# Kernel optimization log

Hardware: AMD Instinct MI355X
Metric: run time of the kernel (lower is better)

## Reference

```python
import jax, jax.numpy as jnp
import numpy as np

P, G, F, H = 128, 256, 1024, 512
EPS = 1e-5

def _bn(x, g, b, m, v):
    # eval-mode BatchNorm1d over last dim
    return (x - m) / jnp.sqrt(v + EPS) * g + b

def _lrelu(x):
    return jnp.where(x > 0, x, 0.1 * x)

def setup_inputs():
    key = jax.random.key(0)
    ks = iter(jax.random.split(key, 64))
    rn = lambda s, sc=1.0: jax.random.normal(next(ks), s, dtype=jnp.float32) * sc
    ru = lambda s: jax.random.uniform(next(ks), s, dtype=jnp.float32) + 0.5
    return {
        "f_p": rn((P, F)), "f_g": rn((G, F)),
        "bn_g": ru((F,)), "bn_b": rn((F,), 0.1), "bn_m": rn((F,), 0.1), "bn_v": ru((F,)),
        "rf_W1": rn((F, F), 0.02), "rf_b1": rn((F,), 0.01),
        "rf1_g": ru((F,)), "rf1_b": rn((F,), 0.1), "rf1_m": rn((F,), 0.1), "rf1_v": ru((F,)),
        "rf_W2": rn((F, F), 0.02), "rf_b2": rn((F,), 0.01),
        "rf2_g": ru((F,)), "rf2_b": rn((F,), 0.1), "rf2_m": rn((F,), 0.1), "rf2_v": ru((F,)),
        "sfc_W": rn((F, H), 0.02), "sfc_b": rn((H,), 0.01),
        "sbn_g": ru((H,)), "sbn_b": rn((H,), 0.1), "sbn_m": rn((H,), 0.1), "sbn_v": ru((H,)),
        "scl_W": rn((H, 1), 0.001), "scl_b": rn((1,), 0.001),
        "ffc_W": rn((F, H), 0.02), "ffc_b": rn((H,), 0.01),
        "fbn_g": ru((H,)), "fbn_b": rn((H,), 0.1), "fbn_m": rn((H,), 0.1), "fbn_v": ru((H,)),
        "cls_W": rn((H, 1), 0.001), "cls_b": rn((1,), 0.001),
    }

def reference(f_p, f_g, bn_g, bn_b, bn_m, bn_v,
              rf_W1, rf_b1, rf1_g, rf1_b, rf1_m, rf1_v,
              rf_W2, rf_b2, rf2_g, rf2_b, rf2_m, rf2_v,
              sfc_W, sfc_b, sbn_g, sbn_b, sbn_m, sbn_v, scl_W, scl_b,
              ffc_W, ffc_b, fbn_g, fbn_b, fbn_m, fbn_v, cls_W, cls_b):
    # Siamese difference feature for every probe-gallery pair: d [P,G,F]
    d = _bn((f_p[:, None, :] - f_g[None, :, :]) ** 2, bn_g, bn_b, bn_m, bn_v)
    h = _lrelu(_bn(d @ rf_W1 + rf_b1, rf1_g, rf1_b, rf1_m, rf1_v))
    t = _lrelu(_bn(h @ rf_W2 + rf_b2, rf2_g, rf2_b, rf2_m, rf2_v))
    # Gallery-gallery scalar affinities via Siamese FcBlock + ClassBlock: w [G,G]
    dg = _bn((f_g[:, None, :] - f_g[None, :, :]) ** 2, bn_g, bn_b, bn_m, bn_v)
    hg = _lrelu(_bn(dg @ sfc_W + sfc_b, sbn_g, sbn_b, sbn_m, sbn_v))
    w = (hg @ scl_W + scl_b)[..., 0]
    # Graph diffusion over the gallery axis: d_new = t @ w  [P,G,F]
    d_new = jnp.einsum('pgf,gh->phf', t, w)
    # Per-pair FC + classifier -> scalar score per (probe, gallery) pair
    feat = _lrelu(_bn(d_new @ ffc_W + ffc_b, fbn_g, fbn_b, fbn_m, fbn_v))
    result = (feat @ cls_W + cls_b)[..., 0]
    return result
```

## Files before the change

kernel.cpp:

```cpp
#include <hip/hip_runtime.h>


typedef __bf16 bf16;
typedef __attribute__((ext_vector_type(8))) __bf16 bf16x8;
typedef __attribute__((ext_vector_type(4))) float f32x4;

#define EPSV 1e-5f

__device__ __forceinline__ void async_load16(const bf16* g, bf16* l) {
    __builtin_amdgcn_global_load_lds(
        (const __attribute__((address_space(1))) void*)g,
        (__attribute__((address_space(3))) void*)l, 16, 0, 0);
}

__global__ __launch_bounds__(256) void prep_kernel(
    const float* __restrict__ g, const float* __restrict__ b,
    const float* __restrict__ m, const float* __restrict__ v,
    const float* __restrict__ bias, float* __restrict__ scale,
    float* __restrict__ offset, int n)
{
    int i = blockIdx.x * 256 + threadIdx.x;
    if (i >= n) return;
    float s = g[i] / sqrtf(v[i] + EPSV);
    float o = b[i] - m[i] * s;
    if (bias) o += bias[i] * s;
    scale[i] = s;
    offset[i] = o;
}

__global__ __launch_bounds__(256) void wtrans_kernel(
    const float* __restrict__ in, bf16* __restrict__ out, int K, int N)
{
    int k = blockIdx.x * 256 + threadIdx.x;
    int n = blockIdx.y;
    out[(size_t)n * K + k] = (bf16)in[(size_t)k * N + n];
}

__global__ __launch_bounds__(256) void wconv_kernel(
    const float* __restrict__ w_acc, const float* __restrict__ sclb,
    bf16* __restrict__ wT)
{
    int tid = blockIdx.x * 256 + threadIdx.x;
    int g2 = tid >> 8, g1 = tid & 255;
    int idx = ((g1 >> 4) <= (g2 >> 4)) ? (g1 * 256 + g2) : (g2 * 256 + g1);
    wT[tid] = (bf16)(w_acc[idx] + sclb[0]);
}

__global__ __launch_bounds__(256) void utrans_kernel(
    const bf16* __restrict__ u, bf16* __restrict__ uT)
{
    __shared__ float tile[64][65];
    int g0 = blockIdx.x * 64, h0 = blockIdx.y * 64, p = blockIdx.z;
    const bf16* up = u + (size_t)p * 256 * 512;
    bf16* op = uT + (size_t)p * 512 * 256;
    for (int c = threadIdx.x; c < 512; c += 256) {
        int r = c >> 3, hc = (c & 7) * 8;
        bf16x8 val = *(const bf16x8*)(up + (size_t)(g0 + r) * 512 + h0 + hc);
#pragma unroll
        for (int j = 0; j < 8; ++j) tile[r][hc + j] = (float)val[j];
    }
    __syncthreads();
    for (int c = threadIdx.x; c < 512; c += 256) {
        int hr = c >> 3, gc = (c & 7) * 8;
        bf16x8 val;
#pragma unroll
        for (int j = 0; j < 8; ++j) val[j] = (bf16)tile[gc + j][hr];
        *(bf16x8*)(op + (size_t)(h0 + hr) * 256 + g0 + gc) = val;
    }
}

__global__ __launch_bounds__(256) void finout_kernel(
    const float* __restrict__ acc, const float* __restrict__ clsb,
    float* __restrict__ out)
{
    int i = blockIdx.x * 256 + threadIdx.x;
    out[i] = acc[i] + clsb[0];
}

__global__ __launch_bounds__(512) void gemm256(
    const bf16* __restrict__ A,
    const float* __restrict__ pairX, const float* __restrict__ pairY,
    const float* __restrict__ ps, const float* __restrict__ po,
    const bf16* __restrict__ BT,
    bf16* __restrict__ C,
    int K, int N, int rowOff,
    const float* __restrict__ scale, const float* __restrict__ offset,
    int lrelu)
{
    __shared__ bf16 As[256 * 64];
    __shared__ bf16 Bs[256 * 64];
    const int tid  = threadIdx.x;
    const int lane = tid & 63;
    const int wave = tid >> 6;
    const int wrow = wave >> 2, wcol = wave & 3;
    const int row0 = blockIdx.y * 256;
    const int col0 = blockIdx.x * 256;
    const int q = lane >> 4, l16 = lane & 15;

    f32x4 acc[8][4];
#pragma unroll
    for (int mi = 0; mi < 8; ++mi)
#pragma unroll
        for (int ni = 0; ni < 4; ++ni)
#pragma unroll
            for (int e = 0; e < 4; ++e) acc[mi][ni][e] = 0.f;

    for (int kk = 0; kk < K; kk += 64) {
        if (pairX) {
#pragma unroll
            for (int t = 0; t < 4; ++t) {
                int c = tid + t * 512;
                int r = c >> 3, ch = c & 7;
                int gr = rowOff + row0 + r;
                const float* xp = pairX + (size_t)(gr >> 8) * K + kk + ch * 8;
                const float* yp = pairY + (size_t)(gr & 255) * K + kk + ch * 8;
                f32x4 x0 = *(const f32x4*)xp, x1 = *(const f32x4*)(xp + 4);
                f32x4 y0 = *(const f32x4*)yp, y1 = *(const f32x4*)(yp + 4);
                f32x4 sa = *(const f32x4*)(ps + kk + ch * 8);
                f32x4 sb = *(const f32x4*)(ps + kk + ch * 8 + 4);
                f32x4 oa = *(const f32x4*)(po + kk + ch * 8);
                f32x4 ob = *(const f32x4*)(po + kk + ch * 8 + 4);
                bf16x8 dv;
#pragma unroll
                for (int j = 0; j < 4; ++j) {
                    float d0 = x0[j] - y0[j];
                    float d1 = x1[j] - y1[j];
                    dv[j]     = (bf16)(d0 * d0 * sa[j] + oa[j]);
                    dv[j + 4] = (bf16)(d1 * d1 * sb[j] + ob[j]);
                }
                *(bf16x8*)&As[r * 64 + ((ch ^ (r & 7)) * 8)] = dv;
            }
        } else {
#pragma unroll
            for (int t = 0; t < 4; ++t) {
                int idx = t * 512 + tid;
                int r = idx >> 3, sch = idx & 7;
                int gch = sch ^ (r & 7);
                async_load16(A + (size_t)(row0 + r) * K + kk + gch * 8,
                             &As[idx * 8]);
            }
        }
#pragma unroll
        for (int t = 0; t < 4; ++t) {
            int idx = t * 512 + tid;
            int r = idx >> 3, sch = idx & 7;
            int gch = sch ^ (r & 7);
            async_load16(BT + (size_t)(col0 + r) * K + kk + gch * 8,
                         &Bs[idx * 8]);
        }
        __syncthreads();

#pragma unroll
        for (int s = 0; s < 2; ++s) {
            bf16x8 af[8], bfr[4];
#pragma unroll
            for (int mi = 0; mi < 8; ++mi) {
                int r = wrow * 128 + mi * 16 + l16;
                af[mi] = *(const bf16x8*)&As[r * 64 + (((s * 4 + q) ^ (r & 7)) * 8)];
            }
#pragma unroll
            for (int ni = 0; ni < 4; ++ni) {
                int rc = wcol * 64 + ni * 16 + l16;
                bfr[ni] = *(const bf16x8*)&Bs[rc * 64 + (((s * 4 + q) ^ (rc & 7)) * 8)];
            }
#pragma unroll
            for (int mi = 0; mi < 8; ++mi)
#pragma unroll
                for (int ni = 0; ni < 4; ++ni)
                    acc[mi][ni] = __builtin_amdgcn_mfma_f32_16x16x32_bf16(
                        af[mi], bfr[ni], acc[mi][ni], 0, 0, 0);
        }
        __syncthreads();
    }

#pragma unroll
    for (int mi = 0; mi < 8; ++mi)
#pragma unroll
        for (int ni = 0; ni < 4; ++ni)
#pragma unroll
            for (int i = 0; i < 4; ++i) {
                int r = row0 + wrow * 128 + mi * 16 + q * 4 + i;
                int cc = col0 + wcol * 64 + ni * 16 + l16;
                float val = acc[mi][ni][i];
                if (scale) val = val * scale[cc] + offset[cc];
                if (lrelu) val = val > 0.f ? val : 0.1f * val;
                C[(size_t)r * N + cc] = (bf16)val;
            }
}

__global__ __launch_bounds__(512) void gemm_aff(
    const float* __restrict__ pairX,
    const float* __restrict__ ps, const float* __restrict__ po,
    const bf16* __restrict__ BT,
    int K,
    const float* __restrict__ scale, const float* __restrict__ offset,
    const float* __restrict__ sclW, float* __restrict__ w_acc)
{
    __shared__ bf16 As[256 * 64];
    __shared__ bf16 Bs[128 * 64];
    const int tid  = threadIdx.x;
    const int lane = tid & 63;
    const int wave = tid >> 6;
    const int wrow = wave >> 1, wcol = wave & 1;
    const int q = lane >> 4, l16 = lane & 15;
    const int col0 = blockIdx.x * 128;

    int ta = 0, rem = blockIdx.y;
    while (rem >= 16 - ta) { rem -= 16 - ta; ++ta; }
    const int tb = ta + rem;

    f32x4 acc[4][4];
#pragma unroll
    for (int mi = 0; mi < 4; ++mi)
#pragma unroll
        for (int ni = 0; ni < 4; ++ni)
#pragma unroll
            for (int e = 0; e < 4; ++e) acc[mi][ni][e] = 0.f;

    for (int kk = 0; kk < K; kk += 64) {
#pragma unroll
        for (int t = 0; t < 4; ++t) {
            int c = tid + t * 512;
            int r = c >> 3, ch = c & 7;
            int g1 = ta * 16 + (r >> 4), g2 = tb * 16 + (r & 15);
            const float* xp = pairX + (size_t)g1 * K + kk + ch * 8;
            const float* yp = pairX + (size_t)g2 * K + kk + ch * 8;
            f32x4 x0 = *(const f32x4*)xp, x1 = *(const f32x4*)(xp + 4);
            f32x4 y0 = *(const f32x4*)yp, y1 = *(const f32x4*)(yp + 4);
            f32x4 sa = *(const f32x4*)(ps + kk + ch * 8);
            f32x4 sb = *(const f32x4*)(ps + kk + ch * 8 + 4);
            f32x4 oa = *(const f32x4*)(po + kk + ch * 8);
            f32x4 ob = *(const f32x4*)(po + kk + ch * 8 + 4);
            bf16x8 dv;
#pragma unroll
            for (int j = 0; j < 4; ++j) {
                float d0 = x0[j] - y0[j];
                float d1 = x1[j] - y1[j];
                dv[j]     = (bf16)(d0 * d0 * sa[j] + oa[j]);
                dv[j + 4] = (bf16)(d1 * d1 * sb[j] + ob[j]);
            }
            *(bf16x8*)&As[r * 64 + ((ch ^ (r & 7)) * 8)] = dv;
        }
#pragma unroll
        for (int t = 0; t < 2; ++t) {
            int idx = t * 512 + tid;
            int r = idx >> 3, sch = idx & 7;
            int gch = sch ^ (r & 7);
            async_load16(BT + (size_t)(col0 + r) * K + kk + gch * 8,
                         &Bs[idx * 8]);
        }
        __syncthreads();

#pragma unroll
        for (int s = 0; s < 2; ++s) {
            bf16x8 af[4], bfr[4];
#pragma unroll
            for (int mi = 0; mi < 4; ++mi) {
                int r = wrow * 64 + mi * 16 + l16;
                af[mi] = *(const bf16x8*)&As[r * 64 + (((s * 4 + q) ^ (r & 7)) * 8)];
            }
#pragma unroll
            for (int ni = 0; ni < 4; ++ni) {
                int rc = wcol * 64 + ni * 16 + l16;
                bfr[ni] = *(const bf16x8*)&Bs[rc * 64 + (((s * 4 + q) ^ (rc & 7)) * 8)];
            }
#pragma unroll
            for (int mi = 0; mi < 4; ++mi)
#pragma unroll
                for (int ni = 0; ni < 4; ++ni)
                    acc[mi][ni] = __builtin_amdgcn_mfma_f32_16x16x32_bf16(
                        af[mi], bfr[ni], acc[mi][ni], 0, 0, 0);
        }
        __syncthreads();
    }

#pragma unroll
    for (int mi = 0; mi < 4; ++mi)
#pragma unroll
        for (int i = 0; i < 4; ++i) {
            float rs = 0.f;
#pragma unroll
            for (int ni = 0; ni < 4; ++ni) {
                int cc = col0 + wcol * 64 + ni * 16 + l16;
                float val = acc[mi][ni][i] * scale[cc] + offset[cc];
                val = val > 0.f ? val : 0.1f * val;
                rs += val * sclW[cc];
            }
            rs += __shfl_xor(rs, 1, 64);
            rs += __shfl_xor(rs, 2, 64);
            rs += __shfl_xor(rs, 4, 64);
            rs += __shfl_xor(rs, 8, 64);
            if (l16 == 0) {
                int r = wrow * 64 + mi * 16 + q * 4 + i;
                int g1 = ta * 16 + (r >> 4), g2 = tb * 16 + (r & 15);
                atomicAdd(w_acc + g1 * 256 + g2, rs);
            }
        }
}

__global__ __launch_bounds__(256) void gemm_kernel(
    const bf16* __restrict__ A,
    const bf16* __restrict__ BT, bf16* __restrict__ C,
    int K, int N, long long batchB, long long batchC,
    const float* __restrict__ scale, const float* __restrict__ offset,
    int lrelu, const float* __restrict__ fuseW, float* __restrict__ facc,
    long long faccStride)
{
    __shared__ bf16 As[128 * 64];
    __shared__ bf16 Bs[128 * 64];
    const int tid  = threadIdx.x;
    const int lane = tid & 63;
    const int wave = tid >> 6;
    const int wr = wave >> 1, wc = wave & 1;
    const int row0 = blockIdx.y * 128;
    const int col0 = blockIdx.x * 128;
    const int q = lane >> 4, l16 = lane & 15;
    const int drow = lane >> 3;
    const int dsch = lane & 7;

    const bf16* Bp = BT + (size_t)blockIdx.z * (size_t)batchB;
    bf16* Cp = C + (size_t)blockIdx.z * (size_t)batchC;

    f32x4 acc[4][4];
#pragma unroll
    for (int mi = 0; mi < 4; ++mi)
#pragma unroll
        for (int ni = 0; ni < 4; ++ni)
#pragma unroll
            for (int e = 0; e < 4; ++e) acc[mi][ni][e] = 0.f;

    for (int kk = 0; kk < K; kk += 64) {
#pragma unroll
        for (int t = 0; t < 4; ++t) {
            int grp = wave * 4 + t;
            int r = grp * 8 + drow;
            int gch = dsch ^ (r & 7);
            async_load16(A + (size_t)(row0 + r) * K + kk + gch * 8,
                         &As[grp * 512 + lane * 8]);
        }
#pragma unroll
        for (int t = 0; t < 4; ++t) {
            int grp = wave * 4 + t;
            int r = grp * 8 + drow;
            int gch = dsch ^ (r & 7);
            async_load16(Bp + (size_t)(col0 + r) * K + kk + gch * 8,
                         &Bs[grp * 512 + lane * 8]);
        }
        __syncthreads();
#pragma unroll
        for (int s = 0; s < 2; ++s) {
            bf16x8 af[4], bfr[4];
#pragma unroll
            for (int mi = 0; mi < 4; ++mi) {
                int r = wr * 64 + mi * 16 + l16;
                af[mi] = *(const bf16x8*)&As[r * 64 + (((s * 4 + q) ^ (r & 7)) * 8)];
            }
#pragma unroll
            for (int ni = 0; ni < 4; ++ni) {
                int rc = wc * 64 + ni * 16 + l16;
                bfr[ni] = *(const bf16x8*)&Bs[rc * 64 + (((s * 4 + q) ^ (rc & 7)) * 8)];
            }
#pragma unroll
            for (int mi = 0; mi < 4; ++mi)
#pragma unroll
                for (int ni = 0; ni < 4; ++ni)
                    acc[mi][ni] = __builtin_amdgcn_mfma_f32_16x16x32_bf16(
                        af[mi], bfr[ni], acc[mi][ni], 0, 0, 0);
        }
        __syncthreads();
    }

    if (fuseW) {
#pragma unroll
        for (int mi = 0; mi < 4; ++mi)
#pragma unroll
            for (int i = 0; i < 4; ++i) {
                float rs = 0.f;
#pragma unroll
                for (int ni = 0; ni < 4; ++ni) {
                    int cc = col0 + wc * 64 + ni * 16 + l16;
                    float val = acc[mi][ni][i] * scale[cc] + offset[cc];
                    val = val > 0.f ? val : 0.1f * val;
                    rs += val * fuseW[cc];
                }
                rs += __shfl_xor(rs, 1, 64);
                rs += __shfl_xor(rs, 2, 64);
                rs += __shfl_xor(rs, 4, 64);
                rs += __shfl_xor(rs, 8, 64);
                if (l16 == 0) {
                    int r = row0 + wr * 64 + mi * 16 + q * 4 + i;
                    atomicAdd(facc + (size_t)blockIdx.z * faccStride + r, rs);
                }
            }
        return;
    }
#pragma unroll
    for (int mi = 0; mi < 4; ++mi)
#pragma unroll
        for (int ni = 0; ni < 4; ++ni)
#pragma unroll
            for (int i = 0; i < 4; ++i) {
                int r = row0 + wr * 64 + mi * 16 + q * 4 + i;
                int cc = col0 + wc * 64 + ni * 16 + l16;
                float val = acc[mi][ni][i];
                if (scale) val = val * scale[cc] + offset[cc];
                if (lrelu) val = val > 0.f ? val : 0.1f * val;
                Cp[(size_t)r * N + cc] = (bf16)val;
            }
}

extern "C" void kernel_launch(void* const* d_in, const int* in_sizes, int n_in,
                              void* d_out, int out_size, void* d_ws, size_t ws_size,
                              hipStream_t stream)
{
    const float* f_p   = (const float*)d_in[0];
    const float* f_g   = (const float*)d_in[1];
    const float* bn_g  = (const float*)d_in[2];
    const float* bn_b  = (const float*)d_in[3];
    const float* bn_m  = (const float*)d_in[4];
    const float* bn_v  = (const float*)d_in[5];
    const float* rf_W1 = (const float*)d_in[6];
    const float* rf_b1 = (const float*)d_in[7];
    const float* rf1_g = (const float*)d_in[8];
    const float* rf1_b = (const float*)d_in[9];
    const float* rf1_m = (const float*)d_in[10];
    const float* rf1_v = (const float*)d_in[11];
    const float* rf_W2 = (const float*)d_in[12];
    const float* rf_b2 = (const float*)d_in[13];
    const float* rf2_g = (const float*)d_in[14];
    const float* rf2_b = (const float*)d_in[15];
    const float* rf2_m = (const float*)d_in[16];
    const float* rf2_v = (const float*)d_in[17];
    const float* sfc_W = (const float*)d_in[18];
    const float* sfc_b = (const float*)d_in[19];
    const float* sbn_g = (const float*)d_in[20];
    const float* sbn_b = (const float*)d_in[21];
    const float* sbn_m = (const float*)d_in[22];
    const float* sbn_v = (const float*)d_in[23];
    const float* scl_W = (const float*)d_in[24];
    const float* scl_b = (const float*)d_in[25];
    const float* ffc_W = (const float*)d_in[26];
    const float* ffc_b = (const float*)d_in[27];
    const float* fbn_g = (const float*)d_in[28];
    const float* fbn_b = (const float*)d_in[29];
    const float* fbn_m = (const float*)d_in[30];
    const float* fbn_v = (const float*)d_in[31];
    const float* cls_W = (const float*)d_in[32];
    const float* cls_b = (const float*)d_in[33];

    const size_t MB = 1ull << 20;
    char* ws = (char*)d_ws;
    float* SC      = (float*)(ws);
    float *s0 = SC,        *o0 = SC + 1024;
    float *s1 = SC + 2048, *o1 = SC + 3072;
    float *s2 = SC + 4096, *o2 = SC + 5120;
    float *s3 = SC + 6144, *o3 = SC + 6656;
    float *s4 = SC + 7168, *o4 = SC + 7680;
    float* w_acc   = (float*)(ws + 65536);
    float* out_acc = (float*)(ws + 327680);
    bf16* wT       = (bf16*)(ws + 458752);
    bf16* W1T      = (bf16*)(ws + 1 * MB);
    bf16* W2T      = (bf16*)(ws + 3 * MB);
    bf16* sfcT     = (bf16*)(ws + 5 * MB);
    bf16* ffcT     = (bf16*)(ws + 6 * MB);

    int nc;
    if      (ws_size >= 170 * MB) nc = 1;
    else if (ws_size >= 90 * MB)  nc = 2;
    else                          nc = 4;
    const int pc = 128 / nc;
    const int R  = pc * 256;
    const size_t hbytes = (size_t)R * 1024 * 2;
    bf16* bufA = (bf16*)(ws + 8 * MB);
    bf16* bufB = (bf16*)(ws + 8 * MB + hbytes);
    bf16* bufC = (bf16*)(ws + 8 * MB + 2 * hbytes);

    prep_kernel<<<dim3(4), 256, 0, stream>>>(bn_g, bn_b, bn_m, bn_v, nullptr, s0, o0, 1024);
    prep_kernel<<<dim3(4), 256, 0, stream>>>(rf1_g, rf1_b, rf1_m, rf1_v, rf_b1, s1, o1, 1024);
    prep_kernel<<<dim3(4), 256, 0, stream>>>(rf2_g, rf2_b, rf2_m, rf2_v, rf_b2, s2, o2, 1024);
    prep_kernel<<<dim3(2), 256, 0, stream>>>(sbn_g, sbn_b, sbn_m, sbn_v, sfc_b, s3, o3, 512);
    prep_kernel<<<dim3(2), 256, 0, stream>>>(fbn_g, fbn_b, fbn_m, fbn_v, ffc_b, s4, o4, 512);

    wtrans_kernel<<<dim3(4, 1024), 256, 0, stream>>>(rf_W1, W1T, 1024, 1024);
    wtrans_kernel<<<dim3(4, 1024), 256, 0, stream>>>(rf_W2, W2T, 1024, 1024);
    wtrans_kernel<<<dim3(4, 512), 256, 0, stream>>>(sfc_W, sfcT, 1024, 512);
    wtrans_kernel<<<dim3(4, 512), 256, 0, stream>>>(ffc_W, ffcT, 1024, 512);

    hipMemsetAsync(ws + 65536, 0, 393216, stream);

    gemm_aff<<<dim3(4, 136), 512, 0, stream>>>(
        f_g, s0, o0, sfcT, 1024, s3, o3, scl_W, w_acc);
    wconv_kernel<<<dim3(256), 256, 0, stream>>>(w_acc, scl_b, wT);

    for (int ci = 0; ci < nc; ++ci) {
        gemm256<<<dim3(4, R / 256), 512, 0, stream>>>(
            nullptr, f_p, f_g, s0, o0, W1T, bufA, 1024, 1024, ci * R,
            s1, o1, 1);
        gemm256<<<dim3(4, R / 256), 512, 0, stream>>>(
            bufA, nullptr, nullptr, nullptr, nullptr, W2T, bufB, 1024, 1024, 0,
            s2, o2, 1);
        gemm256<<<dim3(2, R / 256), 512, 0, stream>>>(
            bufB, nullptr, nullptr, nullptr, nullptr, ffcT, bufC, 1024, 512, 0,
            nullptr, nullptr, 0);
        utrans_kernel<<<dim3(4, 8, pc), 256, 0, stream>>>(bufC, bufA);
        gemm_kernel<<<dim3(4, 2, pc), 256, 0, stream>>>(
            wT, bufA, nullptr, 256, 512, (long long)512 * 256, 0,
            s4, o4, 1, cls_W, out_acc + (size_t)ci * pc * 256, 256);
    }
    finout_kernel<<<dim3(128), 256, 0, stream>>>(out_acc, cls_b, (float*)d_out);
}
```

Baseline: 592.2 us.

## Compute transposed FFC output directly and drop the transpose kernel

The FFC GEMM is recast as ffcT × bufB^T per probe, batched over the probe axis, so it writes the [H,G] layout the diffusion GEMM needs directly. This removes the separate utrans transpose kernel and its extra global round trip. gemm256 gains batch strides and a fused BN+LReLU+classifier row-reduction epilogue, replacing the smaller 128-tile gemm_kernel for the diffusion step. The diffusion GEMM now launches far fewer, larger blocks (2×1×pc), which may lower occupancy.

Result: faster. 566.7 us (-4.3%).

```diff
diff --git a/kernel.cpp b/kernel.cpp
--- a/kernel.cpp
+++ b/kernel.cpp
@@ -46,29 +46,6 @@
     wT[tid] = (bf16)(w_acc[idx] + sclb[0]);
 }
 
-__global__ __launch_bounds__(256) void utrans_kernel(
-    const bf16* __restrict__ u, bf16* __restrict__ uT)
-{
-    __shared__ float tile[64][65];
-    int g0 = blockIdx.x * 64, h0 = blockIdx.y * 64, p = blockIdx.z;
-    const bf16* up = u + (size_t)p * 256 * 512;
-    bf16* op = uT + (size_t)p * 512 * 256;
-    for (int c = threadIdx.x; c < 512; c += 256) {
-        int r = c >> 3, hc = (c & 7) * 8;
-        bf16x8 val = *(const bf16x8*)(up + (size_t)(g0 + r) * 512 + h0 + hc);
-#pragma unroll
-        for (int j = 0; j < 8; ++j) tile[r][hc + j] = (float)val[j];
-    }
-    __syncthreads();
-    for (int c = threadIdx.x; c < 512; c += 256) {
-        int hr = c >> 3, gc = (c & 7) * 8;
-        bf16x8 val;
-#pragma unroll
-        for (int j = 0; j < 8; ++j) val[j] = (bf16)tile[gc + j][hr];
-        *(bf16x8*)(op + (size_t)(h0 + hr) * 256 + g0 + gc) = val;
-    }
-}
-
 __global__ __launch_bounds__(256) void finout_kernel(
     const float* __restrict__ acc, const float* __restrict__ clsb,
     float* __restrict__ out)
@@ -84,8 +61,11 @@
     const bf16* __restrict__ BT,
     bf16* __restrict__ C,
     int K, int N, int rowOff,
+    long long batchA, long long batchB, long long batchC,
     const float* __restrict__ scale, const float* __restrict__ offset,
-    int lrelu)
+    int lrelu,
+    const float* __restrict__ fuseW, float* __restrict__ facc,
+    long long faccStride)
 {
     __shared__ bf16 As[256 * 64];
     __shared__ bf16 Bs[256 * 64];
@@ -96,6 +76,10 @@
     const int row0 = blockIdx.y * 256;
     const int col0 = blockIdx.x * 256;
     const int q = lane >> 4, l16 = lane & 15;
+    const int z = blockIdx.z;
+
+    const bf16* Ap = A + (size_t)z * (size_t)batchA;
+    const bf16* Bp = BT + (size_t)z * (size_t)batchB;
 
     f32x4 acc[8][4];
 #pragma unroll
@@ -136,7 +120,7 @@
                 int idx = t * 512 + tid;
                 int r = idx >> 3, sch = idx & 7;
                 int gch = sch ^ (r & 7);
-                async_load16(A + (size_t)(row0 + r) * K + kk + gch * 8,
+                async_load16(Ap + (size_t)(row0 + r) * K + kk + gch * 8,
                              &As[idx * 8]);
             }
         }
@@ -145,7 +129,7 @@
             int idx = t * 512 + tid;
             int r = idx >> 3, sch = idx & 7;
             int gch = sch ^ (r & 7);
-            async_load16(BT + (size_t)(col0 + r) * K + kk + gch * 8,
+            async_load16(Bp + (size_t)(col0 + r) * K + kk + gch * 8,
                          &Bs[idx * 8]);
         }
         __syncthreads();
@@ -173,6 +157,31 @@
         __syncthreads();
     }
 
+    if (fuseW) {
+#pragma unroll
+        for (int mi = 0; mi < 8; ++mi)
+#pragma unroll
+            for (int i = 0; i < 4; ++i) {
+                float rs = 0.f;
+#pragma unroll
+                for (int ni = 0; ni < 4; ++ni) {
+                    int cc = col0 + wcol * 64 + ni * 16 + l16;
+                    float val = acc[mi][ni][i] * scale[cc] + offset[cc];
+                    val = val > 0.f ? val : 0.1f * val;
+                    rs += val * fuseW[cc];
+                }
+                rs += __shfl_xor(rs, 1, 64);
+                rs += __shfl_xor(rs, 2, 64);
+                rs += __shfl_xor(rs, 4, 64);
+                rs += __shfl_xor(rs, 8, 64);
+                if (l16 == 0) {
+                    int r = row0 + wrow * 128 + mi * 16 + q * 4 + i;
+                    atomicAdd(facc + (size_t)z * faccStride + r, rs);
+                }
+            }
+        return;
+    }
+    bf16* Cp = C + (size_t)z * (size_t)batchC;
 #pragma unroll
     for (int mi = 0; mi < 8; ++mi)
 #pragma unroll
@@ -184,7 +193,7 @@
                 float val = acc[mi][ni][i];
                 if (scale) val = val * scale[cc] + offset[cc];
                 if (lrelu) val = val > 0.f ? val : 0.1f * val;
-                C[(size_t)r * N + cc] = (bf16)val;
+                Cp[(size_t)r * N + cc] = (bf16)val;
             }
 }
 
@@ -296,117 +305,6 @@
                 atomicAdd(w_acc + g1 * 256 + g2, rs);
             }
         }
-}
-
-__global__ __launch_bounds__(256) void gemm_kernel(
-    const bf16* __restrict__ A,
-    const bf16* __restrict__ BT, bf16* __restrict__ C,
-    int K, int N, long long batchB, long long batchC,
-    const float* __restrict__ scale, const float* __restrict__ offset,
-    int lrelu, const float* __restrict__ fuseW, float* __restrict__ facc,
-    long long faccStride)
-{
-    __shared__ bf16 As[128 * 64];
-    __shared__ bf16 Bs[128 * 64];
-    const int tid  = threadIdx.x;
-    const int lane = tid & 63;
-    const int wave = tid >> 6;
-    const int wr = wave >> 1, wc = wave & 1;
-    const int row0 = blockIdx.y * 128;
-    const int col0 = blockIdx.x * 128;
-    const int q = lane >> 4, l16 = lane & 15;
-    const int drow = lane >> 3;
-    const int dsch = lane & 7;
-
-    const bf16* Bp = BT + (size_t)blockIdx.z * (size_t)batchB;
-    bf16* Cp = C + (size_t)blockIdx.z * (size_t)batchC;
-
-    f32x4 acc[4][4];
-#pragma unroll
-    for (int mi = 0; mi < 4; ++mi)
-#pragma unroll
-        for (int ni = 0; ni < 4; ++ni)
-#pragma unroll
-            for (int e = 0; e < 4; ++e) acc[mi][ni][e] = 0.f;
-
-    for (int kk = 0; kk < K; kk += 64) {
-#pragma unroll
-        for (int t = 0; t < 4; ++t) {
-            int grp = wave * 4 + t;
-            int r = grp * 8 + drow;
-            int gch = dsch ^ (r & 7);
-            async_load16(A + (size_t)(row0 + r) * K + kk + gch * 8,
-                         &As[grp * 512 + lane * 8]);
-        }
-#pragma unroll
-        for (int t = 0; t < 4; ++t) {
-            int grp = wave * 4 + t;
-            int r = grp * 8 + drow;
-            int gch = dsch ^ (r & 7);
-            async_load16(Bp + (size_t)(col0 + r) * K + kk + gch * 8,
-                         &Bs[grp * 512 + lane * 8]);
-        }
-        __syncthreads();
-#pragma unroll
-        for (int s = 0; s < 2; ++s) {
-            bf16x8 af[4], bfr[4];
-#pragma unroll
-            for (int mi = 0; mi < 4; ++mi) {
-                int r = wr * 64 + mi * 16 + l16;
-                af[mi] = *(const bf16x8*)&As[r * 64 + (((s * 4 + q) ^ (r & 7)) * 8)];
-            }
-#pragma unroll
-            for (int ni = 0; ni < 4; ++ni) {
-                int rc = wc * 64 + ni * 16 + l16;
-                bfr[ni] = *(const bf16x8*)&Bs[rc * 64 + (((s * 4 + q) ^ (rc & 7)) * 8)];
-            }
-#pragma unroll
-            for (int mi = 0; mi < 4; ++mi)
-#pragma unroll
-                for (int ni = 0; ni < 4; ++ni)
-                    acc[mi][ni] = __builtin_amdgcn_mfma_f32_16x16x32_bf16(
-                        af[mi], bfr[ni], acc[mi][ni], 0, 0, 0);
-        }
-        __syncthreads();
-    }
-
-    if (fuseW) {
-#pragma unroll
-        for (int mi = 0; mi < 4; ++mi)
-#pragma unroll
-            for (int i = 0; i < 4; ++i) {
-                float rs = 0.f;
-#pragma unroll
-                for (int ni = 0; ni < 4; ++ni) {
-                    int cc = col0 + wc * 64 + ni * 16 + l16;
-                    float val = acc[mi][ni][i] * scale[cc] + offset[cc];
-                    val = val > 0.f ? val : 0.1f * val;
-                    rs += val * fuseW[cc];
-                }
-                rs += __shfl_xor(rs, 1, 64);
-                rs += __shfl_xor(rs, 2, 64);
-                rs += __shfl_xor(rs, 4, 64);
-                rs += __shfl_xor(rs, 8, 64);
-                if (l16 == 0) {
-                    int r = row0 + wr * 64 + mi * 16 + q * 4 + i;
-                    atomicAdd(facc + (size_t)blockIdx.z * faccStride + r, rs);
-                }
-            }
-        return;
-    }
-#pragma unroll
-    for (int mi = 0; mi < 4; ++mi)
-#pragma unroll
-        for (int ni = 0; ni < 4; ++ni)
-#pragma unroll
-            for (int i = 0; i < 4; ++i) {
-                int r = row0 + wr * 64 + mi * 16 + q * 4 + i;
-                int cc = col0 + wc * 64 + ni * 16 + l16;
-                float val = acc[mi][ni][i];
-                if (scale) val = val * scale[cc] + offset[cc];
-                if (lrelu) val = val > 0.f ? val : 0.1f * val;
-                Cp[(size_t)r * N + cc] = (bf16)val;
-            }
 }
 
 extern "C" void kernel_launch(void* const* d_in, const int* in_sizes, int n_in,
@@ -495,16 +393,17 @@
     for (int ci = 0; ci < nc; ++ci) {
         gemm256<<<dim3(4, R / 256), 512, 0, stream>>>(
             nullptr, f_p, f_g, s0, o0, W1T, bufA, 1024, 1024, ci * R,
-            s1, o1, 1);
+            0, 0, 0, s1, o1, 1, nullptr, nullptr, 0);
         gemm256<<<dim3(4, R / 256), 512, 0, stream>>>(
             bufA, nullptr, nullptr, nullptr, nullptr, W2T, bufB, 1024, 1024, 0,
-            s2, o2, 1);
-        gemm256<<<dim3(2, R / 256), 512, 0, stream>>>(
-            bufB, nullptr, nullptr, nullptr, nullptr, ffcT, bufC, 1024, 512, 0,
-            nullptr, nullptr, 0);
-        utrans_kernel<<<dim3(4, 8, pc), 256, 0, stream>>>(bufC, bufA);
-        gemm_kernel<<<dim3(4, 2, pc), 256, 0, stream>>>(
-            wT, bufA, nullptr, 256, 512, (long long)512 * 256, 0,
+            0, 0, 0, s2, o2, 1, nullptr, nullptr, 0);
+        gemm256<<<dim3(1, 2, pc), 512, 0, stream>>>(
+            ffcT, nullptr, nullptr, nullptr, nullptr, bufB, bufC, 1024, 256, 0,
+            0, (long long)256 * 1024, (long long)512 * 256,
+            nullptr, nullptr, 0, nullptr, nullptr, 0);
+        gemm256<<<dim3(2, 1, pc), 512, 0, stream>>>(
+            wT, nullptr, nullptr, nullptr, nullptr, bufC, nullptr, 256, 512, 0,
+            0, (long long)512 * 256, 0,
             s4, o4, 1, cls_W, out_acc + (size_t)ci * pc * 256, 256);
     }
     finout_kernel<<<dim3(128), 256, 0, stream>>>(out_acc, cls_b, (float*)d_out);
```
